# Optimization experiments

Measured on AMD Instinct MI355X. Metric: run time of the kernel, lower is better.

The kernel has to match this reference:

```python
import jax, jax.numpy as jnp
import numpy as np

NUM_COEFF = 32   # num_coeff_per_dim
NUM_POINTS = 64  # Chebyshev collocation points
MAX_ITERS = 10
TOL = 0.01
BATCH, DIM, HID, T_EVAL_N = 512, 256, 512, 16


def T_grid(t, n):
    # Chebyshev T_k(t), k=0..n-1 -> [n, len(t)]
    rows = [jnp.ones_like(t), t]
    for _ in range(2, n):
        rows.append(2.0 * t * rows[-1] - rows[-2])
    return jnp.stack(rows[:n])


def U_grid(t, n):
    rows = [jnp.ones_like(t), 2.0 * t]
    for _ in range(2, n):
        rows.append(2.0 * t * rows[-1] - rows[-2])
    return jnp.stack(rows[:n])


def DT_grid(t, n):
    # d/dt T_k = k * U_{k-1}
    return jnp.vstack([jnp.zeros((1, t.shape[0]), t.dtype),
                       U_grid(t, n - 1) * jnp.arange(1, n, dtype=t.dtype)[:, None]])


def vf_point(t, y, W1, b1, W2, b2):
    # f(t, y) for y [B, D], scalar t
    h = jnp.tanh(y @ W1 + b1 + t)
    return h @ W2 + b2


def vf_grid(t, y, W1, b1, W2, b2):
    # vectorized over Chebyshev points: y [B, D, P], t [P]
    h = jnp.tanh(jnp.einsum('bdp,dh->bhp', y, W1) + b1[None, :, None] + t[None, None, :])
    return jnp.einsum('bhp,hd->bdp', h, W2) + b2[None, :, None]


def setup_inputs() -> dict:
    key = jax.random.key(0)
    ks = jax.random.split(key, 7)
    s1 = 1.0 / np.sqrt(DIM)
    s2 = 1.0 / np.sqrt(HID)
    return {
        'y_init': jax.random.normal(ks[0], (BATCH, DIM), jnp.float32),
        't_eval': jnp.linspace(0.0, 1.0, T_EVAL_N, dtype=jnp.float32),
        'B_init': jax.random.uniform(ks[1], (BATCH, DIM, NUM_COEFF - 2), jnp.float32),
        'W1': jax.random.normal(ks[2], (DIM, HID), jnp.float32) * s1,
        'b1': jax.random.normal(ks[3], (HID,), jnp.float32) * 0.1,
        'W2': jax.random.normal(ks[4], (HID, DIM), jnp.float32) * s2,
        'b2': jax.random.normal(ks[5], (DIM,), jnp.float32) * 0.1,
    }


def _pan_solve(y_init, t_eval, B_init, W1, b1, W2, b2):
    t0, t1 = t_eval[0], t_eval[-1]
    dt = t_eval.dtype
    # time-independent spectral operators
    t_cheb = -jnp.sign(t1 - t0) * jnp.cos(jnp.pi * jnp.arange(NUM_POINTS, dtype=dt) / NUM_POINTS)
    Dt = jnp.diff(jnp.concatenate([t_cheb, jnp.ones((1,), dt)]))
    Phi = T_grid(t_cheb, NUM_COEFF)                        # [N, P]
    DPhi = (2.0 / (t1 - t0)) * DT_grid(t_cheb, NUM_COEFF)  # [N, P]
    inv0 = jnp.linalg.inv(jnp.stack([Phi[0:2, 0], DPhi[0:2, 0]]).T)  # [2,2]
    PD2 = jnp.stack([Phi[2:, 0], DPhi[2:, 0]], axis=-1)    # [N-2, 2]
    D01 = jnp.stack([DPhi[0, :], DPhi[1, :]], axis=0)      # [2, P]
    Phi_b = DPhi[2:, :] - PD2 @ inv0 @ D01                 # [N-2, P]
    Q = jnp.linalg.inv(Phi_b @ (Dt[:, None] * Phi_b.T))    # [N-2, N-2]
    PhibTQ = (Dt[:, None] * Phi_b.T) @ Q                   # [P, N-2]
    M2 = inv0 @ D01 @ PhibTQ                               # [2, N-2]

    f_init = vf_point(t0, y_init, W1, b1, W2, b2)
    yf2 = jnp.stack([y_init, f_init], axis=-1)             # [B, D, 2]

    def head(B_tail):
        return (yf2 - B_tail @ PD2) @ inv0                 # [B, D, 2]

    B = B_init
    done = jnp.array(False)
    delta = jnp.array(jnp.inf, dt)
    iters = jnp.array(0, jnp.int32)
    for _ in range(MAX_ITERS):  # Picard fixed-point iteration (masked early stop)
        B_prev = B
        B_full = jnp.concatenate([head(B_prev), B_prev], axis=-1)  # [B, D, N]
        y_grid = jnp.einsum('bdn,np->bdp', B_full, Phi)            # [B, D, P]
        fapprox = vf_grid(t_cheb, y_grid, W1, b1, W2, b2)          # [B, D, P]
        B_new = jnp.einsum('bdp,pn->bdn', fapprox, PhibTQ) - yf2 @ M2
        d = jnp.linalg.norm(B_new - B_prev)
        B = jnp.where(done, B_prev, B_new)
        delta = jnp.where(done, delta, d)
        iters = jnp.where(done, iters, iters + 1)
        done = done | (d < TOL)

    B_full = jnp.concatenate([head(B), B], axis=-1)
    t_out = -1.0 + 2.0 * (t_eval - t0) / (t1 - t0)
    Phi_out = T_grid(t_out, NUM_COEFF)                     # [N, T]
    traj = jnp.einsum('bdn,nt->tbd', B_full, Phi_out)      # [T, B, D]
    return traj, B, delta, iters


def reference(y_init, t_eval, B_init, W1, b1, W2, b2):
    traj, B, delta, iters = _pan_solve(y_init, t_eval, B_init, W1, b1, W2, b2)
    return (t_eval, traj, delta, B)
```

## Files before the change

### kernel.cpp

```cpp
#include <hip/hip_runtime.h>
#include <math.h>

#define NBATCH 512
#define NDIM 256
#define NHID 512
#define NC 32
#define NTAIL 30
#define NP 64
#define TEV 16
#define MAXIT 10
#define TOLF 0.01f
#define PI_F 3.14159265358979323846f

typedef __bf16 bf16_t;
typedef __bf16 bf16x8 __attribute__((ext_vector_type(8)));
typedef float f32x4 __attribute__((ext_vector_type(4)));
typedef unsigned short ushort_t;

constexpr size_t OFF_TCHEB = 0;
constexpr size_t OFF_PHIT  = 64;
constexpr size_t OFF_PD2I  = 2112;
constexpr size_t OFF_M2    = 2176;
constexpr size_t OFF_INV0  = 2240;
constexpr size_t OFF_PHIOUT= 2256;
constexpr size_t OFF_PQ    = 2768;
constexpr size_t OFF_PQBH  = 4816;
constexpr size_t OFF_PQBL  = 5840;
constexpr size_t OFF_PHIH  = 6864;
constexpr size_t OFF_PHIL  = 7888;
constexpr size_t OFF_SCAL  = 8912;
constexpr size_t OFF_H1F   = 8928;
constexpr size_t OFF_YF2I  = OFF_H1F + 262144;
constexpr size_t OFF_YFR   = OFF_YF2I + 262144;
constexpr size_t OFF_BT    = OFF_YFR + 3932160;
constexpr size_t OFF_W1T   = OFF_BT + 3932160;
constexpr size_t OFF_W2T   = OFF_W1T + 65536;
constexpr size_t WS_FLOATS = OFF_W2T + 65536;

constexpr size_t OUT_TEVAL = 0;
constexpr size_t OUT_TRAJ  = 16;
constexpr size_t OUT_DELTA = 16 + (size_t)TEV*NBATCH*NDIM;
constexpr size_t OUT_B     = OUT_DELTA + 1;

__device__ __forceinline__ ushort_t bf16bits(float v) {
    bf16_t h = (bf16_t)v; ushort_t u; __builtin_memcpy(&u, &h, 2); return u;
}
__device__ __forceinline__ float bf16val(ushort_t u) {
    bf16_t h; __builtin_memcpy(&h, &u, 2); return (float)h;
}

__global__ void setup_kernel(const float* __restrict__ t_eval, float* __restrict__ ws,
                             float* __restrict__ out)
{
    __shared__ float Phi[32][64];
    __shared__ float DPhi[32][64];
    __shared__ float Phib[30][64];
    __shared__ float tcs[64];
    __shared__ float DtS[64];
    __shared__ float inv0s[4];
    __shared__ float pd2s[30][2];
    __shared__ double Gaug[30][61];
    __shared__ double rowk[60];
    __shared__ double colk[30];

    const int tid = threadIdx.x;
    const float t0 = t_eval[0], t1 = t_eval[TEV-1];
    const float sgn = (t1 > t0) ? 1.f : -1.f;

    if (tid < 64) {
        const float t = -sgn * cosf(PI_F * (float)tid / 64.f);
        tcs[tid] = t;
        float p0 = 1.f, p1 = t;
        Phi[0][tid] = p0; Phi[1][tid] = p1;
        for (int k = 2; k < 32; ++k) { float pk = 2.f*t*p1 - p0; Phi[k][tid] = pk; p0 = p1; p1 = pk; }
        const float sc = 2.f / (t1 - t0);
        float u0 = 1.f, u1 = 2.f*t;
        DPhi[0][tid] = 0.f;
        DPhi[1][tid] = sc * 1.f * u0;
        DPhi[2][tid] = sc * 2.f * u1;
        for (int k = 3; k < 32; ++k) { float uk = 2.f*t*u1 - u0; DPhi[k][tid] = sc * (float)k * uk; u0 = u1; u1 = uk; }
    }
    __syncthreads();
    if (tid < 64) DtS[tid] = ((tid < 63) ? tcs[tid+1] : 1.0f) - tcs[tid];
    if (tid == 0) {
        double a = Phi[0][0], b = DPhi[0][0], c = Phi[1][0], d = DPhi[1][0];
        double det = a*d - b*c;
        inv0s[0] = (float)( d/det); inv0s[1] = (float)(-b/det);
        inv0s[2] = (float)(-c/det); inv0s[3] = (float)( a/det);
    }
    __syncthreads();
    if (tid == 0) { ws[OFF_INV0+0]=inv0s[0]; ws[OFF_INV0+1]=inv0s[1]; ws[OFF_INV0+2]=inv0s[2]; ws[OFF_INV0+3]=inv0s[3]; }
    if (tid < 30) {
        float P = Phi[2+tid][0], D = DPhi[2+tid][0];
        float a0 = P*inv0s[0] + D*inv0s[2];
        float a1 = P*inv0s[1] + D*inv0s[3];
        pd2s[tid][0] = a0; pd2s[tid][1] = a1;
        ws[OFF_PD2I + tid*2+0] = a0;
        ws[OFF_PD2I + tid*2+1] = a1;
    }
    __syncthreads();
    if (tid < 64)
        for (int m = 0; m < 30; ++m)
            Phib[m][tid] = DPhi[2+m][tid] - (pd2s[m][0]*DPhi[0][tid] + pd2s[m][1]*DPhi[1][tid]);
    __syncthreads();

    for (int e = tid; e < 900; e += 256) {
        int i = e / 30, j = e % 30;
        double s = 0.0;
        for (int p = 0; p < 64; ++p) s += (double)Phib[i][p] * (double)DtS[p] * (double)Phib[j][p];
        Gaug[i][j] = s;
        Gaug[i][30+j] = (i == j) ? 1.0 : 0.0;
    }
    __syncthreads();

    for (int k = 0; k < 30; ++k) {
        double invpv = 1.0 / Gaug[k][k];
        if (tid < 60) rowk[tid] = Gaug[k][tid] * invpv;
        if (tid >= 64 && tid < 94) colk[tid-64] = Gaug[tid-64][k];
        __syncthreads();
        for (int e = tid; e < 1800; e += 256) {
            int i = e / 60, j = e - i*60;
            if (i == k) Gaug[i][j] = rowk[j];
            else        Gaug[i][j] -= colk[i] * rowk[j];
        }
        __syncthreads();
    }

    if (tid < 64) {
        ushort_t* pqh = (ushort_t*)(ws + OFF_PQBH);
        ushort_t* pql = (ushort_t*)(ws + OFF_PQBL);
        float pqrow[32];
        for (int n = 0; n < 30; ++n) {
            double s = 0.0;
            for (int m = 0; m < 30; ++m) s += (double)Phib[m][tid] * Gaug[m][30+n];
            pqrow[n] = (float)((double)DtS[tid] * s);
        }
        pqrow[30] = 0.f; pqrow[31] = 0.f;
        for (int n = 0; n < 32; ++n) {
            ws[OFF_PQ + (size_t)tid*32 + n] = pqrow[n];
            bf16_t h = (bf16_t)pqrow[n];
            float hf = (float)h;
            pqh[n*64 + tid] = bf16bits(pqrow[n]);
            pql[n*64 + tid] = bf16bits(pqrow[n] - hf);
        }
    }
    __syncthreads();

    if (tid < 30) {
        double a20 = 0.0, a21 = 0.0;
        for (int p = 0; p < 64; ++p) {
            double pq = (double)ws[OFF_PQ + (size_t)p*32 + tid];
            a20 += (double)DPhi[0][p] * pq;
            a21 += (double)DPhi[1][p] * pq;
        }
        ws[OFF_M2 + 0*32 + tid] = (float)((double)inv0s[0]*a20 + (double)inv0s[1]*a21);
        ws[OFF_M2 + 1*32 + tid] = (float)((double)inv0s[2]*a20 + (double)inv0s[3]*a21);
    }

    if (tid < 64) {
        ushort_t* phh = (ushort_t*)(ws + OFF_PHIH);
        ushort_t* phl = (ushort_t*)(ws + OFF_PHIL);
        for (int n = 0; n < 32; ++n) {
            float f = Phi[n][tid];
            ws[OFF_PHIT + (size_t)tid*32 + n] = f;
            ushort_t hb = bf16bits(f);
            phh[tid*32 + n] = hb;
            phl[tid*32 + n] = bf16bits(f - bf16val(hb));
        }
        ws[OFF_TCHEB + tid] = tcs[tid];
    }

    if (tid < TEV) {
        float te = t_eval[tid];
        out[OUT_TEVAL + tid] = te;
        float tt = -1.f + 2.f*(te - t0)/(t1 - t0);
        float q0 = 1.f, q1 = tt;
        ws[OFF_PHIOUT + (size_t)tid*32 + 0] = q0;
        ws[OFF_PHIOUT + (size_t)tid*32 + 1] = q1;
        for (int k = 2; k < 32; ++k) { float qk = 2.f*tt*q1 - q0; ws[OFF_PHIOUT + (size_t)tid*32 + k] = qk; q0 = q1; q1 = qk; }
    }

    if (tid == 0) {
        double* acc = (double*)(ws + OFF_SCAL);
        acc[0] = 0.0;
        int* ip = (int*)(ws + OFF_SCAL + 2);
        ip[0] = 0;
        ip[1] = 0;
    }
}

__global__ __launch_bounds__(256) void transB_kernel(const float* __restrict__ Bin, float* __restrict__ Bt)
{
    const int t = threadIdx.x, b = blockIdx.x;
    const float* src = Bin + ((size_t)(b*NDIM + t)) * NTAIL;
    #pragma unroll
    for (int n = 0; n < NTAIL; ++n)
        Bt[((size_t)b*NTAIL + n)*NDIM + t] = src[n];
}

__global__ __launch_bounds__(256) void transW_kernel(const float* __restrict__ W, bf16_t* __restrict__ Wt,
                                                     int R, int C)
{
    __shared__ float Ls[64][65];
    const int r0 = blockIdx.x*64, c0 = blockIdx.y*64;
    const int lr = threadIdx.x >> 6, lc = threadIdx.x & 63;
    #pragma unroll
    for (int i = 0; i < 16; ++i) {
        int rr = i*4 + lr;
        Ls[rr][lc] = W[(size_t)(r0+rr)*C + c0+lc];
    }
    __syncthreads();
    #pragma unroll
    for (int i = 0; i < 16; ++i) {
        int cc = i*4 + lr;
        Wt[(size_t)(c0+cc)*R + r0 + lc] = (bf16_t)Ls[lc][cc];
    }
}

__global__ __launch_bounds__(512) void finit_h_kernel(const float* __restrict__ y, const float* __restrict__ W1,
                                                      const float* __restrict__ b1, const float* __restrict__ t_eval,
                                                      float* __restrict__ h1)
{
    __shared__ float ys[NDIM];
    const int t = threadIdx.x, b = blockIdx.x;
    if (t < NDIM) ys[t] = y[(size_t)b*NDIM + t];
    __syncthreads();
    float acc = b1[t] + t_eval[0];
    for (int d = 0; d < NDIM; ++d) acc += ys[d] * W1[(size_t)d*NHID + t];
    h1[(size_t)b*NHID + t] = tanhf(acc);
}

__global__ __launch_bounds__(256) void finit_rest_kernel(const float* __restrict__ y, const float* __restrict__ W2,
                                                         const float* __restrict__ b2, const float* __restrict__ h1,
                                                         const float* __restrict__ inv0,
                                                         float* __restrict__ yf2i, float* __restrict__ yfr)
{
    __shared__ float hs[NHID];
    const int t = threadIdx.x, b = blockIdx.x;
    hs[t] = h1[(size_t)b*NHID + t];
    hs[t+256] = h1[(size_t)b*NHID + 256 + t];
    __syncthreads();
    float f = b2[t];
    for (int h = 0; h < NHID; ++h) f += hs[h] * W2[(size_t)h*NDIM + t];
    const float yv = y[(size_t)b*NDIM + t];
    yf2i[((size_t)b*2 + 0)*NDIM + t] = yv*inv0[0] + f*inv0[2];
    yf2i[((size_t)b*2 + 1)*NDIM + t] = yv*inv0[1] + f*inv0[3];
    yfr[((size_t)b*2 + 0)*NDIM + t] = yv;
    yfr[((size_t)b*2 + 1)*NDIM + t] = f;
}

__global__ __launch_bounds__(512, 4) void iter_kernel(
    const float* __restrict__ pd2i, const float* __restrict__ yf2i, const float* __restrict__ tch,
    const bf16_t* __restrict__ W1t, const bf16_t* __restrict__ W2t,
    const float* __restrict__ b1f, const float* __restrict__ b2f,
    const ushort_t* __restrict__ PQhi, const ushort_t* __restrict__ PQlo,
    const ushort_t* __restrict__ phiH, const ushort_t* __restrict__ phiL,
    const float* __restrict__ yfr, const float* __restrict__ M2f,
    float* __restrict__ Bt,
    double* __restrict__ accum, int* __restrict__ counter,
    int* __restrict__ done, float* __restrict__ outDelta)
{
    if (*done) return;
    __shared__ float pd2s[32][2];
    __shared__ float tchS[64];
    __shared__ float m2S[64];
    __shared__ double redd[8];
    __shared__ __align__(16) char smemA[33792];
    __shared__ __align__(16) char smemB[17408];
    __shared__ __align__(16) ushort_t PQHs[32*72];
    __shared__ __align__(16) ushort_t PQLs[32*72];

    const int t = threadIdx.x;
    const int b = blockIdx.x;
    const int lane = t & 63, w = t >> 6;
    const int fr = lane & 15, quad = lane >> 4;

    if (t < 60) ((float*)pd2s)[t] = pd2i[t];
    if (t >= 64 && t < 128) tchS[t-64] = tch[t-64];
    if (t >= 128 && t < 192) m2S[t-128] = M2f[t-128];
    __syncthreads();

    if (t < 256) {
        float cf[32];
        #pragma unroll
        for (int n = 0; n < NTAIL; ++n) cf[2+n] = Bt[((size_t)b*NTAIL + n)*NDIM + t];
        float c0 = yf2i[((size_t)b*2 + 0)*NDIM + t];
        float c1 = yf2i[((size_t)b*2 + 1)*NDIM + t];
        #pragma unroll
        for (int n = 0; n < NTAIL; ++n) { c0 -= cf[2+n]*pd2s[n][0]; c1 -= cf[2+n]*pd2s[n][1]; }
        cf[0] = c0; cf[1] = c1;
        unsigned* BH32 = (unsigned*)smemA;
        unsigned* BL32 = (unsigned*)(smemA + 16384);
        #pragma unroll
        for (int n2 = 0; n2 < 16; ++n2) {
            float f0 = cf[2*n2], f1 = cf[2*n2+1];
            ushort_t h0 = bf16bits(f0), h1 = bf16bits(f1);
            ushort_t l0 = bf16bits(f0 - bf16val(h0)), l1 = bf16bits(f1 - bf16val(h1));
            int idx = t*16 + ((n2 >> 2) ^ (t & 3))*4 + (n2 & 3);
            BH32[idx] = (unsigned)h0 | ((unsigned)h1 << 16);
            BL32[idx] = (unsigned)l0 | ((unsigned)l1 << 16);
        }
    } else {
        int e = (t - 256) * 8;
        int r = e >> 6, c = e & 63;
        uint4 vh = *(const uint4*)(PQhi + e);
        uint4 vl = *(const uint4*)(PQlo + e);
        *(uint4*)(PQHs + r*72 + c) = vh;
        *(uint4*)(PQLs + r*72 + c) = vl;
    }
    __syncthreads();

    ushort_t* Ay = (ushort_t*)smemA;
    {
        bf16x8 bH[2], bL[2];
        const ushort_t* BHu = (const ushort_t*)smemA;
        const ushort_t* BLu = (const ushort_t*)(smemA + 16384);
        #pragma unroll
        for (int j = 0; j < 2; ++j) {
            const int d = w*32 + j*16 + fr;
            const int off = d*32 + (quad ^ (d & 3))*8;
            bH[j] = *(const bf16x8*)(BHu + off);
            bL[j] = *(const bf16x8*)(BLu + off);
        }
        bf16x8 aH[4], aL[4];
        #pragma unroll
        for (int i = 0; i < 4; ++i) {
            aH[i] = *(const bf16x8*)(phiH + (i*16 + fr)*32 + quad*8);
            aL[i] = *(const bf16x8*)(phiL + (i*16 + fr)*32 + quad*8);
        }
        __syncthreads();
        f32x4 accY[4][2];
        #pragma unroll
        for (int i = 0; i < 4; ++i)
            #pragma unroll
            for (int j = 0; j < 2; ++j) {
                f32x4 a = (f32x4){0.f,0.f,0.f,0.f};
                a = __builtin_amdgcn_mfma_f32_16x16x32_bf16(aH[i], bH[j], a, 0, 0, 0);
                a = __builtin_amdgcn_mfma_f32_16x16x32_bf16(aH[i], bL[j], a, 0, 0, 0);
                a = __builtin_amdgcn_mfma_f32_16x16x32_bf16(aL[i], bH[j], a, 0, 0, 0);
                accY[i][j] = a;
            }
        #pragma unroll
        for (int i = 0; i < 4; ++i)
            #pragma unroll
            for (int j = 0; j < 2; ++j)
                #pragma unroll
                for (int r = 0; r < 4; ++r) {
                    const int p = i*16 + quad*4 + r;
                    const int d = w*32 + j*16 + fr;
                    Ay[p*264 + d] = bf16bits(accY[i][j][r]);
                }
    }
    __syncthreads();

    ushort_t* Hc = (ushort_t*)smemB;
    f32x4 accF[4][2];
    #pragma unroll
    for (int i = 0; i < 4; ++i)
        #pragma unroll
        for (int j = 0; j < 2; ++j) accF[i][j] = (f32x4){0.f,0.f,0.f,0.f};

    #pragma unroll
    for (int pass = 0; pass < 4; ++pass) {
        bf16x8 w2f[4][2];
        #pragma unroll
        for (int kt4 = 0; kt4 < 4; ++kt4)
            #pragma unroll
            for (int j = 0; j < 2; ++j) {
                const int d = w*32 + j*16 + fr;
                w2f[kt4][j] = *(const bf16x8*)(W2t + (size_t)d*NHID + pass*128 + kt4*32 + quad*8);
            }
        f32x4 acc1[4];
        #pragma unroll
        for (int i = 0; i < 4; ++i) acc1[i] = (f32x4){0.f,0.f,0.f,0.f};
        #pragma unroll
        for (int kt = 0; kt < NDIM; kt += 32) {
            bf16x8 af[4], bfv;
            #pragma unroll
            for (int i = 0; i < 4; ++i)
                af[i] = *(const bf16x8*)(Ay + (i*16 + fr)*264 + kt + quad*8);
            {
                const int ncol = pass*128 + w*16 + fr;
                bfv = *(const bf16x8*)(W1t + (size_t)ncol*NDIM + kt + quad*8);
            }
            #pragma unroll
            for (int i = 0; i < 4; ++i)
                acc1[i] = __builtin_amdgcn_mfma_f32_16x16x32_bf16(af[i], bfv, acc1[i], 0, 0, 0);
        }
        __syncthreads();
        {
            const int col = w*16 + fr;
            const float bv = b1f[pass*128 + col];
            #pragma unroll
            for (int i = 0; i < 4; ++i)
                #pragma unroll
                for (int r = 0; r < 4; ++r) {
                    const int row = i*16 + quad*4 + r;
                    float v = acc1[i][r] + bv + tchS[row];
                    v = fminf(fmaxf(v, -15.f), 15.f);
                    float e = __expf(2.f*v);
                    Hc[row*136 + col] = bf16bits((e - 1.f)/(e + 1.f));
                }
        }
        __syncthreads();
        #pragma unroll
        for (int kt4 = 0; kt4 < 4; ++kt4) {
            bf16x8 af[4];
            #pragma unroll
            for (int i = 0; i < 4; ++i)
                af[i] = *(const bf16x8*)(Hc + (i*16 + fr)*136 + kt4*32 + quad*8);
            #pragma unroll
            for (int i = 0; i < 4; ++i)
                #pragma unroll
                for (int j = 0; j < 2; ++j)
                    accF[i][j] = __builtin_amdgcn_mfma_f32_16x16x32_bf16(af[i], w2f[kt4][j], accF[i][j], 0, 0, 0);
        }
    }
    __syncthreads();

    {
        unsigned* FsT32 = (unsigned*)smemA;
        #pragma unroll
        for (int i = 0; i < 4; ++i)
            #pragma unroll
            for (int j = 0; j < 2; ++j) {
                const int d = w*32 + j*16 + fr;
                const float bv = b2f[d];
                #pragma unroll
                for (int rp = 0; rp < 2; ++rp) {
                    unsigned u0 = bf16bits(accF[i][j][rp*2]   + bv);
                    unsigned u1 = bf16bits(accF[i][j][rp*2+1] + bv);
                    FsT32[d*33 + i*8 + quad*2 + rp] = u0 | (u1 << 16);
                }
            }
    }
    __syncthreads();

    double ss = 0.0;
    {
        const ushort_t* FsTu = (const ushort_t*)smemA;
        float yvv[2], ffv[2];
        #pragma unroll
        for (int j2 = 0; j2 < 2; ++j2) {
            const int d2 = w*32 + j2*16 + fr;
            yvv[j2] = yfr[((size_t)b*2 + 0)*NDIM + d2];
            ffv[j2] = yfr[((size_t)b*2 + 1)*NDIM + d2];
        }
        f32x4 acc2[2][2];
        #pragma unroll
        for (int m2 = 0; m2 < 2; ++m2)
            #pragma unroll
            for (int j2 = 0; j2 < 2; ++j2) acc2[m2][j2] = (f32x4){0.f,0.f,0.f,0.f};
        #pragma unroll
        for (int kk = 0; kk < 2; ++kk) {
            bf16x8 ah[2], al[2];
            #pragma unroll
            for (int m2 = 0; m2 < 2; ++m2) {
                const int off = (m2*16 + fr)*72 + kk*32 + quad*8;
                ah[m2] = *(const bf16x8*)(PQHs + off);
                al[m2] = *(const bf16x8*)(PQLs + off);
            }
            #pragma unroll
            for (int j2 = 0; j2 < 2; ++j2) {
                const int d2 = w*32 + j2*16 + fr;
                bf16x8 bfv = *(const bf16x8*)(FsTu + d2*66 + kk*32 + quad*8);
                #pragma unroll
                for (int m2 = 0; m2 < 2; ++m2) {
                    acc2[m2][j2] = __builtin_amdgcn_mfma_f32_16x16x32_bf16(ah[m2], bfv, acc2[m2][j2], 0, 0, 0);
                    acc2[m2][j2] = __builtin_amdgcn_mfma_f32_16x16x32_bf16(al[m2], bfv, acc2[m2][j2], 0, 0, 0);
                }
            }
        }
        #pragma unroll
        for (int m2 = 0; m2 < 2; ++m2)
            #pragma unroll
            for (int j2 = 0; j2 < 2; ++j2)
                #pragma unroll
                for (int rr = 0; rr < 4; ++rr) {
                    const int n = m2*16 + quad*4 + rr;
                    if (n < NTAIL) {
                        const int d = w*32 + j2*16 + fr;
                        const size_t idx = ((size_t)b*NTAIL + n)*NDIM + d;
                        float ym2v = yvv[j2]*m2S[n] + ffv[j2]*m2S[32 + n];
                        float val = acc2[m2][j2][rr] - ym2v;
                        float old = Bt[idx];
                        float diff = val - old;
                        Bt[idx] = val;
                        ss += (double)diff*(double)diff;
                    }
                }
    }

    #pragma unroll
    for (int off = 32; off > 0; off >>= 1) ss += __shfl_down(ss, off, 64);
    if (lane == 0) redd[w] = ss;
    __syncthreads();
    if (t == 0) {
        double tot = redd[0] + redd[1] + redd[2] + redd[3]
                   + redd[4] + redd[5] + redd[6] + redd[7];
        atomicAdd(accum, tot);
        __threadfence();
        int old = atomicAdd(counter, 1);
        if (old == 511) {
            unsigned long long raw = atomicExch((unsigned long long*)accum, 0ull);
            double total; __builtin_memcpy(&total, &raw, 8);
            float dl = (float)sqrt(total);
            *outDelta = dl;
            *counter = 0;
            if (dl < TOLF) *done = 1;
        }
    }
}

__global__ __launch_bounds__(256) void kernelEpi(const float* __restrict__ PhiOut, const float* __restrict__ pd2i,
                                                 const float* __restrict__ yf2i, const float* __restrict__ Bt,
                                                 float* __restrict__ outTraj, float* __restrict__ outB)
{
    __shared__ float Po[16][32];
    const int t = threadIdx.x, b = blockIdx.x;
    for (int i = t; i < 512; i += 256) ((float*)Po)[i] = PhiOut[i];
    __syncthreads();
    float cf[32];
    #pragma unroll
    for (int n = 0; n < NTAIL; ++n) cf[2+n] = Bt[((size_t)b*NTAIL + n)*NDIM + t];
    float c0 = yf2i[((size_t)b*2 + 0)*NDIM + t];
    float c1 = yf2i[((size_t)b*2 + 1)*NDIM + t];
    #pragma unroll
    for (int n = 0; n < NTAIL; ++n) { c0 -= cf[2+n]*pd2i[n*2]; c1 -= cf[2+n]*pd2i[n*2+1]; }
    cf[0] = c0; cf[1] = c1;
    for (int tt = 0; tt < TEV; ++tt) {
        float s = 0.f;
        #pragma unroll
        for (int k = 0; k < 32; ++k) s += cf[k]*Po[tt][k];
        outTraj[((size_t)tt*NBATCH + b)*NDIM + t] = s;
    }
    float* ob = outB + ((size_t)(b*NDIM + t))*NTAIL;
    #pragma unroll
    for (int n = 0; n < NTAIL; ++n) ob[n] = cf[2+n];
}

extern "C" void kernel_launch(void* const* d_in, const int* in_sizes, int n_in,
                              void* d_out, int out_size, void* d_ws, size_t ws_size,
                              hipStream_t stream)
{
    const float* y_init = (const float*)d_in[0];
    const float* t_eval = (const float*)d_in[1];
    const float* B_init = (const float*)d_in[2];
    const float* W1     = (const float*)d_in[3];
    const float* b1     = (const float*)d_in[4];
    const float* W2     = (const float*)d_in[5];
    const float* b2     = (const float*)d_in[6];
    float* out = (float*)d_out;
    float* ws  = (float*)d_ws;
    if (ws_size < WS_FLOATS * sizeof(float)) return;

    float* tcheb = ws + OFF_TCHEB;
    float* pd2i  = ws + OFF_PD2I;
    float* M2    = ws + OFF_M2;
    float* inv0  = ws + OFF_INV0;
    float* PhiOut= ws + OFF_PHIOUT;
    double* accum = (double*)(ws + OFF_SCAL);
    int* done    = (int*)(ws + OFF_SCAL + 2);
    int* counter = (int*)(ws + OFF_SCAL + 3);
    float* h1   = ws + OFF_H1F;
    float* yf2i = ws + OFF_YF2I;
    float* yfr  = ws + OFF_YFR;
    float* Bt   = ws + OFF_BT;
    bf16_t* W1t = (bf16_t*)(ws + OFF_W1T);
    bf16_t* W2t = (bf16_t*)(ws + OFF_W2T);
    ushort_t* pqh = (ushort_t*)(ws + OFF_PQBH);
    ushort_t* pql = (ushort_t*)(ws + OFF_PQBL);
    ushort_t* phh = (ushort_t*)(ws + OFF_PHIH);
    ushort_t* phl = (ushort_t*)(ws + OFF_PHIL);

    setup_kernel<<<1, 256, 0, stream>>>(t_eval, ws, out);
    transB_kernel<<<NBATCH, 256, 0, stream>>>(B_init, Bt);
    transW_kernel<<<dim3(NDIM/64, NHID/64), 256, 0, stream>>>(W1, W1t, NDIM, NHID);
    transW_kernel<<<dim3(NHID/64, NDIM/64), 256, 0, stream>>>(W2, W2t, NHID, NDIM);
    finit_h_kernel<<<NBATCH, 512, 0, stream>>>(y_init, W1, b1, t_eval, h1);
    finit_rest_kernel<<<NBATCH, 256, 0, stream>>>(y_init, W2, b2, h1, inv0, yf2i, yfr);

    for (int it = 0; it < MAXIT; ++it) {
        iter_kernel<<<NBATCH, 512, 0, stream>>>(pd2i, yf2i, tcheb, W1t, W2t, b1, b2,
                                                pqh, pql, phh, phl, yfr, M2, Bt,
                                                accum, counter, done, out + OUT_DELTA);
    }
    kernelEpi<<<NBATCH, 256, 0, stream>>>(PhiOut, pd2i, yf2i, Bt, out + OUT_TRAJ, out + OUT_B);
}
```

Baseline: 705.2 us.

## Merge six prologue kernels into one role-dispatched launch

Replaces the setup, B transpose, two weight transposes and the two initial vector-field kernels with a single kernel whose blocks pick a role from blockIdx. The f(t0,y0) evaluation is fused into one block per batch row, and the 2x2 inverse is recomputed in closed form so it no longer waits on the setup block. This removes five launch gaps and the h1 round trip through global memory. In exchange the single setup block, with its serial Gauss-Jordan loop, now runs alongside the other roles, and every block reserves 40 KB of shared memory at 512 threads, which may cut occupancy for the light roles.

```diff
diff --git a/kernel.cpp b/kernel.cpp
--- a/kernel.cpp
+++ b/kernel.cpp
@@ -49,204 +49,217 @@
     bf16_t h; __builtin_memcpy(&h, &u, 2); return (float)h;
 }
 
-__global__ void setup_kernel(const float* __restrict__ t_eval, float* __restrict__ ws,
-                             float* __restrict__ out)
+__global__ __launch_bounds__(512) void prologue_kernel(
+    const float* __restrict__ t_eval, const float* __restrict__ y,
+    const float* __restrict__ Bin,
+    const float* __restrict__ W1, const float* __restrict__ b1,
+    const float* __restrict__ W2, const float* __restrict__ b2,
+    float* __restrict__ ws, float* __restrict__ out)
 {
-    __shared__ float Phi[32][64];
-    __shared__ float DPhi[32][64];
-    __shared__ float Phib[30][64];
-    __shared__ float tcs[64];
-    __shared__ float DtS[64];
-    __shared__ float inv0s[4];
-    __shared__ float pd2s[30][2];
-    __shared__ double Gaug[30][61];
-    __shared__ double rowk[60];
-    __shared__ double colk[30];
+    struct SetupSh {
+        double Gaug[30][61];
+        double rowk[60];
+        double colk[30];
+        float Phi[32][64];
+        float DPhi[32][64];
+        float Phib[30][64];
+        float tcs[64];
+        float DtS[64];
+        float inv0s[4];
+        float pd2s[30][2];
+    };
+    __shared__ __align__(16) char pm[40960];
+    static_assert(sizeof(SetupSh) <= 40960, "SetupSh too big");
 
     const int tid = threadIdx.x;
-    const float t0 = t_eval[0], t1 = t_eval[TEV-1];
-    const float sgn = (t1 > t0) ? 1.f : -1.f;
-
-    if (tid < 64) {
-        const float t = -sgn * cosf(PI_F * (float)tid / 64.f);
-        tcs[tid] = t;
-        float p0 = 1.f, p1 = t;
-        Phi[0][tid] = p0; Phi[1][tid] = p1;
-        for (int k = 2; k < 32; ++k) { float pk = 2.f*t*p1 - p0; Phi[k][tid] = pk; p0 = p1; p1 = pk; }
-        const float sc = 2.f / (t1 - t0);
-        float u0 = 1.f, u1 = 2.f*t;
-        DPhi[0][tid] = 0.f;
-        DPhi[1][tid] = sc * 1.f * u0;
-        DPhi[2][tid] = sc * 2.f * u1;
-        for (int k = 3; k < 32; ++k) { float uk = 2.f*t*u1 - u0; DPhi[k][tid] = sc * (float)k * uk; u0 = u1; u1 = uk; }
-    }
-    __syncthreads();
-    if (tid < 64) DtS[tid] = ((tid < 63) ? tcs[tid+1] : 1.0f) - tcs[tid];
-    if (tid == 0) {
-        double a = Phi[0][0], b = DPhi[0][0], c = Phi[1][0], d = DPhi[1][0];
-        double det = a*d - b*c;
-        inv0s[0] = (float)( d/det); inv0s[1] = (float)(-b/det);
-        inv0s[2] = (float)(-c/det); inv0s[3] = (float)( a/det);
-    }
-    __syncthreads();
-    if (tid == 0) { ws[OFF_INV0+0]=inv0s[0]; ws[OFF_INV0+1]=inv0s[1]; ws[OFF_INV0+2]=inv0s[2]; ws[OFF_INV0+3]=inv0s[3]; }
-    if (tid < 30) {
-        float P = Phi[2+tid][0], D = DPhi[2+tid][0];
-        float a0 = P*inv0s[0] + D*inv0s[2];
-        float a1 = P*inv0s[1] + D*inv0s[3];
-        pd2s[tid][0] = a0; pd2s[tid][1] = a1;
-        ws[OFF_PD2I + tid*2+0] = a0;
-        ws[OFF_PD2I + tid*2+1] = a1;
-    }
-    __syncthreads();
-    if (tid < 64)
-        for (int m = 0; m < 30; ++m)
-            Phib[m][tid] = DPhi[2+m][tid] - (pd2s[m][0]*DPhi[0][tid] + pd2s[m][1]*DPhi[1][tid]);
-    __syncthreads();
-
-    for (int e = tid; e < 900; e += 256) {
-        int i = e / 30, j = e % 30;
-        double s = 0.0;
-        for (int p = 0; p < 64; ++p) s += (double)Phib[i][p] * (double)DtS[p] * (double)Phib[j][p];
-        Gaug[i][j] = s;
-        Gaug[i][30+j] = (i == j) ? 1.0 : 0.0;
-    }
-    __syncthreads();
-
-    for (int k = 0; k < 30; ++k) {
-        double invpv = 1.0 / Gaug[k][k];
-        if (tid < 60) rowk[tid] = Gaug[k][tid] * invpv;
-        if (tid >= 64 && tid < 94) colk[tid-64] = Gaug[tid-64][k];
-        __syncthreads();
-        for (int e = tid; e < 1800; e += 256) {
-            int i = e / 60, j = e - i*60;
-            if (i == k) Gaug[i][j] = rowk[j];
-            else        Gaug[i][j] -= colk[i] * rowk[j];
-        }
-        __syncthreads();
-    }
-
-    if (tid < 64) {
-        ushort_t* pqh = (ushort_t*)(ws + OFF_PQBH);
-        ushort_t* pql = (ushort_t*)(ws + OFF_PQBL);
-        float pqrow[32];
-        for (int n = 0; n < 30; ++n) {
+    const int role = blockIdx.x;
+
+    if (role == 0) {
+        SetupSh& S = *(SetupSh*)pm;
+        const float t0 = t_eval[0], t1 = t_eval[TEV-1];
+        const float sgn = (t1 > t0) ? 1.f : -1.f;
+
+        if (tid < 64) {
+            const float t = -sgn * cosf(PI_F * (float)tid / 64.f);
+            S.tcs[tid] = t;
+            float p0 = 1.f, p1 = t;
+            S.Phi[0][tid] = p0; S.Phi[1][tid] = p1;
+            for (int k = 2; k < 32; ++k) { float pk = 2.f*t*p1 - p0; S.Phi[k][tid] = pk; p0 = p1; p1 = pk; }
+            const float sc = 2.f / (t1 - t0);
+            float u0 = 1.f, u1 = 2.f*t;
+            S.DPhi[0][tid] = 0.f;
+            S.DPhi[1][tid] = sc * 1.f * u0;
+            S.DPhi[2][tid] = sc * 2.f * u1;
+            for (int k = 3; k < 32; ++k) { float uk = 2.f*t*u1 - u0; S.DPhi[k][tid] = sc * (float)k * uk; u0 = u1; u1 = uk; }
+        }
+        __syncthreads();
+        if (tid < 64) S.DtS[tid] = ((tid < 63) ? S.tcs[tid+1] : 1.0f) - S.tcs[tid];
+        if (tid == 0) {
+            double a = S.Phi[0][0], b = S.DPhi[0][0], c = S.Phi[1][0], d = S.DPhi[1][0];
+            double det = a*d - b*c;
+            S.inv0s[0] = (float)( d/det); S.inv0s[1] = (float)(-b/det);
+            S.inv0s[2] = (float)(-c/det); S.inv0s[3] = (float)( a/det);
+        }
+        __syncthreads();
+        if (tid < 30) {
+            float P = S.Phi[2+tid][0], D = S.DPhi[2+tid][0];
+            float a0 = P*S.inv0s[0] + D*S.inv0s[2];
+            float a1 = P*S.inv0s[1] + D*S.inv0s[3];
+            S.pd2s[tid][0] = a0; S.pd2s[tid][1] = a1;
+            ws[OFF_PD2I + tid*2+0] = a0;
+            ws[OFF_PD2I + tid*2+1] = a1;
+        }
+        __syncthreads();
+        if (tid < 64)
+            for (int m = 0; m < 30; ++m)
+                S.Phib[m][tid] = S.DPhi[2+m][tid] - (S.pd2s[m][0]*S.DPhi[0][tid] + S.pd2s[m][1]*S.DPhi[1][tid]);
+        __syncthreads();
+
+        for (int e = tid; e < 900; e += 512) {
+            int i = e / 30, j = e % 30;
             double s = 0.0;
-            for (int m = 0; m < 30; ++m) s += (double)Phib[m][tid] * Gaug[m][30+n];
-            pqrow[n] = (float)((double)DtS[tid] * s);
-        }
-        pqrow[30] = 0.f; pqrow[31] = 0.f;
-        for (int n = 0; n < 32; ++n) {
-            ws[OFF_PQ + (size_t)tid*32 + n] = pqrow[n];
-            bf16_t h = (bf16_t)pqrow[n];
-            float hf = (float)h;
-            pqh[n*64 + tid] = bf16bits(pqrow[n]);
-            pql[n*64 + tid] = bf16bits(pqrow[n] - hf);
-        }
-    }
-    __syncthreads();
-
-    if (tid < 30) {
-        double a20 = 0.0, a21 = 0.0;
-        for (int p = 0; p < 64; ++p) {
-            double pq = (double)ws[OFF_PQ + (size_t)p*32 + tid];
-            a20 += (double)DPhi[0][p] * pq;
-            a21 += (double)DPhi[1][p] * pq;
-        }
-        ws[OFF_M2 + 0*32 + tid] = (float)((double)inv0s[0]*a20 + (double)inv0s[1]*a21);
-        ws[OFF_M2 + 1*32 + tid] = (float)((double)inv0s[2]*a20 + (double)inv0s[3]*a21);
-    }
-
-    if (tid < 64) {
-        ushort_t* phh = (ushort_t*)(ws + OFF_PHIH);
-        ushort_t* phl = (ushort_t*)(ws + OFF_PHIL);
-        for (int n = 0; n < 32; ++n) {
-            float f = Phi[n][tid];
-            ws[OFF_PHIT + (size_t)tid*32 + n] = f;
-            ushort_t hb = bf16bits(f);
-            phh[tid*32 + n] = hb;
-            phl[tid*32 + n] = bf16bits(f - bf16val(hb));
-        }
-        ws[OFF_TCHEB + tid] = tcs[tid];
-    }
-
-    if (tid < TEV) {
-        float te = t_eval[tid];
-        out[OUT_TEVAL + tid] = te;
-        float tt = -1.f + 2.f*(te - t0)/(t1 - t0);
-        float q0 = 1.f, q1 = tt;
-        ws[OFF_PHIOUT + (size_t)tid*32 + 0] = q0;
-        ws[OFF_PHIOUT + (size_t)tid*32 + 1] = q1;
-        for (int k = 2; k < 32; ++k) { float qk = 2.f*tt*q1 - q0; ws[OFF_PHIOUT + (size_t)tid*32 + k] = qk; q0 = q1; q1 = qk; }
-    }
-
-    if (tid == 0) {
-        double* acc = (double*)(ws + OFF_SCAL);
-        acc[0] = 0.0;
-        int* ip = (int*)(ws + OFF_SCAL + 2);
-        ip[0] = 0;
-        ip[1] = 0;
-    }
-}
-
-__global__ __launch_bounds__(256) void transB_kernel(const float* __restrict__ Bin, float* __restrict__ Bt)
-{
-    const int t = threadIdx.x, b = blockIdx.x;
-    const float* src = Bin + ((size_t)(b*NDIM + t)) * NTAIL;
-    #pragma unroll
-    for (int n = 0; n < NTAIL; ++n)
-        Bt[((size_t)b*NTAIL + n)*NDIM + t] = src[n];
-}
-
-__global__ __launch_bounds__(256) void transW_kernel(const float* __restrict__ W, bf16_t* __restrict__ Wt,
-                                                     int R, int C)
-{
-    __shared__ float Ls[64][65];
-    const int r0 = blockIdx.x*64, c0 = blockIdx.y*64;
-    const int lr = threadIdx.x >> 6, lc = threadIdx.x & 63;
-    #pragma unroll
-    for (int i = 0; i < 16; ++i) {
-        int rr = i*4 + lr;
-        Ls[rr][lc] = W[(size_t)(r0+rr)*C + c0+lc];
-    }
-    __syncthreads();
-    #pragma unroll
-    for (int i = 0; i < 16; ++i) {
-        int cc = i*4 + lr;
-        Wt[(size_t)(c0+cc)*R + r0 + lc] = (bf16_t)Ls[lc][cc];
-    }
-}
-
-__global__ __launch_bounds__(512) void finit_h_kernel(const float* __restrict__ y, const float* __restrict__ W1,
-                                                      const float* __restrict__ b1, const float* __restrict__ t_eval,
-                                                      float* __restrict__ h1)
-{
-    __shared__ float ys[NDIM];
-    const int t = threadIdx.x, b = blockIdx.x;
-    if (t < NDIM) ys[t] = y[(size_t)b*NDIM + t];
-    __syncthreads();
-    float acc = b1[t] + t_eval[0];
-    for (int d = 0; d < NDIM; ++d) acc += ys[d] * W1[(size_t)d*NHID + t];
-    h1[(size_t)b*NHID + t] = tanhf(acc);
-}
-
-__global__ __launch_bounds__(256) void finit_rest_kernel(const float* __restrict__ y, const float* __restrict__ W2,
-                                                         const float* __restrict__ b2, const float* __restrict__ h1,
-                                                         const float* __restrict__ inv0,
-                                                         float* __restrict__ yf2i, float* __restrict__ yfr)
-{
-    __shared__ float hs[NHID];
-    const int t = threadIdx.x, b = blockIdx.x;
-    hs[t] = h1[(size_t)b*NHID + t];
-    hs[t+256] = h1[(size_t)b*NHID + 256 + t];
-    __syncthreads();
-    float f = b2[t];
-    for (int h = 0; h < NHID; ++h) f += hs[h] * W2[(size_t)h*NDIM + t];
-    const float yv = y[(size_t)b*NDIM + t];
-    yf2i[((size_t)b*2 + 0)*NDIM + t] = yv*inv0[0] + f*inv0[2];
-    yf2i[((size_t)b*2 + 1)*NDIM + t] = yv*inv0[1] + f*inv0[3];
-    yfr[((size_t)b*2 + 0)*NDIM + t] = yv;
-    yfr[((size_t)b*2 + 1)*NDIM + t] = f;
+            for (int p = 0; p < 64; ++p) s += (double)S.Phib[i][p] * (double)S.DtS[p] * (double)S.Phib[j][p];
+            S.Gaug[i][j] = s;
+            S.Gaug[i][30+j] = (i == j) ? 1.0 : 0.0;
+        }
+        __syncthreads();
+
+        for (int k = 0; k < 30; ++k) {
+            double invpv = 1.0 / S.Gaug[k][k];
+            if (tid < 60) S.rowk[tid] = S.Gaug[k][tid] * invpv;
+            if (tid >= 64 && tid < 94) S.colk[tid-64] = S.Gaug[tid-64][k];
+            __syncthreads();
+            for (int e = tid; e < 1800; e += 512) {
+                int i = e / 60, j = e - i*60;
+                if (i == k) S.Gaug[i][j] = S.rowk[j];
+                else        S.Gaug[i][j] -= S.colk[i] * S.rowk[j];
+            }
+            __syncthreads();
+        }
+
+        if (tid < 64) {
+            ushort_t* pqh = (ushort_t*)(ws + OFF_PQBH);
+            ushort_t* pql = (ushort_t*)(ws + OFF_PQBL);
+            float pqrow[32];
+            for (int n = 0; n < 30; ++n) {
+                double s = 0.0;
+                for (int m = 0; m < 30; ++m) s += (double)S.Phib[m][tid] * S.Gaug[m][30+n];
+                pqrow[n] = (float)((double)S.DtS[tid] * s);
+            }
+            pqrow[30] = 0.f; pqrow[31] = 0.f;
+            for (int n = 0; n < 32; ++n) {
+                ws[OFF_PQ + (size_t)tid*32 + n] = pqrow[n];
+                bf16_t h = (bf16_t)pqrow[n];
+                float hf = (float)h;
+                pqh[n*64 + tid] = bf16bits(pqrow[n]);
+                pql[n*64 + tid] = bf16bits(pqrow[n] - hf);
+            }
+        }
+        __syncthreads();
+
+        if (tid < 30) {
+            double a20 = 0.0, a21 = 0.0;
+            for (int p = 0; p < 64; ++p) {
+                double pq = (double)ws[OFF_PQ + (size_t)p*32 + tid];
+                a20 += (double)S.DPhi[0][p] * pq;
+                a21 += (double)S.DPhi[1][p] * pq;
+            }
+            ws[OFF_M2 + 0*32 + tid] = (float)((double)S.inv0s[0]*a20 + (double)S.inv0s[1]*a21);
+            ws[OFF_M2 + 1*32 + tid] = (float)((double)S.inv0s[2]*a20 + (double)S.inv0s[3]*a21);
+        }
+
+        if (tid < 64) {
+            ushort_t* phh = (ushort_t*)(ws + OFF_PHIH);
+            ushort_t* phl = (ushort_t*)(ws + OFF_PHIL);
+            for (int n = 0; n < 32; ++n) {
+                float f = S.Phi[n][tid];
+                ws[OFF_PHIT + (size_t)tid*32 + n] = f;
+                ushort_t hb = bf16bits(f);
+                phh[tid*32 + n] = hb;
+                phl[tid*32 + n] = bf16bits(f - bf16val(hb));
+            }
+            ws[OFF_TCHEB + tid] = S.tcs[tid];
+        }
+
+        if (tid < TEV) {
+            float te = t_eval[tid];
+            out[OUT_TEVAL + tid] = te;
+            float tt = -1.f + 2.f*(te - t0)/(t1 - t0);
+            float q0 = 1.f, q1 = tt;
+            ws[OFF_PHIOUT + (size_t)tid*32 + 0] = q0;
+            ws[OFF_PHIOUT + (size_t)tid*32 + 1] = q1;
+            for (int k = 2; k < 32; ++k) { float qk = 2.f*tt*q1 - q0; ws[OFF_PHIOUT + (size_t)tid*32 + k] = qk; q0 = q1; q1 = qk; }
+        }
+
+        if (tid == 0) {
+            double* acc = (double*)(ws + OFF_SCAL);
+            acc[0] = 0.0;
+            int* ip = (int*)(ws + OFF_SCAL + 2);
+            ip[0] = 0;
+            ip[1] = 0;
+        }
+    } else if (role <= NBATCH) {
+        const int b = role - 1;
+        float* ys = (float*)pm;
+        float* hs = (float*)pm + 256;
+        if (tid < NDIM) ys[tid] = y[(size_t)b*NDIM + tid];
+        __syncthreads();
+        {
+            float acc = b1[tid] + t_eval[0];
+            for (int d = 0; d < NDIM; ++d) acc += ys[d] * W1[(size_t)d*NHID + tid];
+            hs[tid] = tanhf(acc);
+        }
+        __syncthreads();
+        if (tid < NDIM) {
+            float f = b2[tid];
+            for (int h = 0; h < NHID; ++h) f += hs[h] * W2[(size_t)h*NDIM + tid];
+            const float yv = ys[tid];
+            const float t0 = t_eval[0], t1 = t_eval[TEV-1];
+            const float sgn = (t1 > t0) ? 1.f : -1.f;
+            const float sc = 2.f / (t1 - t0);
+            double a = 1.0, bb = 0.0, c = (double)(-sgn), d = (double)sc;
+            double det = a*d - bb*c;
+            const float i0 = (float)( d/det), i1 = (float)(-bb/det);
+            const float i2 = (float)(-c/det), i3 = (float)( a/det);
+            float* yf2i = ws + OFF_YF2I;
+            float* yfr  = ws + OFF_YFR;
+            yf2i[((size_t)b*2 + 0)*NDIM + tid] = yv*i0 + f*i2;
+            yf2i[((size_t)b*2 + 1)*NDIM + tid] = yv*i1 + f*i3;
+            yfr [((size_t)b*2 + 0)*NDIM + tid] = yv;
+            yfr [((size_t)b*2 + 1)*NDIM + tid] = f;
+        }
+    } else if (role <= 2*NBATCH) {
+        if (tid < NDIM) {
+            const int b = role - NBATCH - 1;
+            float* Bt = ws + OFF_BT;
+            const float* src = Bin + ((size_t)(b*NDIM + tid)) * NTAIL;
+            #pragma unroll
+            for (int n = 0; n < NTAIL; ++n)
+                Bt[((size_t)b*NTAIL + n)*NDIM + tid] = src[n];
+        }
+    } else {
+        const bool isW1 = (role <= 2*NBATCH + 32);
+        const int idx = isW1 ? (role - 2*NBATCH - 1) : (role - 2*NBATCH - 33);
+        const int R = isW1 ? NDIM : NHID;
+        const int C = isW1 ? NHID : NDIM;
+        const float* W = isW1 ? W1 : W2;
+        bf16_t* Wt = (bf16_t*)(ws + (isW1 ? OFF_W1T : OFF_W2T));
+        const int nbx = R / 64;
+        const int r0 = (idx % nbx) * 64, c0 = (idx / nbx) * 64;
+        float (*Ls)[65] = (float(*)[65])pm;
+        const int lr = tid >> 6, lc = tid & 63;
+        #pragma unroll
+        for (int i = 0; i < 8; ++i) {
+            int rr = i*8 + lr;
+            Ls[rr][lc] = W[(size_t)(r0+rr)*C + c0+lc];
+        }
+        __syncthreads();
+        #pragma unroll
+        for (int i = 0; i < 8; ++i) {
+            int cc = i*8 + lr;
+            Wt[(size_t)(c0+cc)*R + r0 + lc] = (bf16_t)Ls[lc][cc];
+        }
+    }
 }
 
 __global__ __launch_bounds__(512, 4) void iter_kernel(
@@ -557,12 +570,10 @@
     float* tcheb = ws + OFF_TCHEB;
     float* pd2i  = ws + OFF_PD2I;
     float* M2    = ws + OFF_M2;
-    float* inv0  = ws + OFF_INV0;
     float* PhiOut= ws + OFF_PHIOUT;
     double* accum = (double*)(ws + OFF_SCAL);
     int* done    = (int*)(ws + OFF_SCAL + 2);
     int* counter = (int*)(ws + OFF_SCAL + 3);
-    float* h1   = ws + OFF_H1F;
     float* yf2i = ws + OFF_YF2I;
     float* yfr  = ws + OFF_YFR;
     float* Bt   = ws + OFF_BT;
@@ -573,12 +584,8 @@
     ushort_t* phh = (ushort_t*)(ws + OFF_PHIH);
     ushort_t* phl = (ushort_t*)(ws + OFF_PHIL);
 
-    setup_kernel<<<1, 256, 0, stream>>>(t_eval, ws, out);
-    transB_kernel<<<NBATCH, 256, 0, stream>>>(B_init, Bt);
-    transW_kernel<<<dim3(NDIM/64, NHID/64), 256, 0, stream>>>(W1, W1t, NDIM, NHID);
-    transW_kernel<<<dim3(NHID/64, NDIM/64), 256, 0, stream>>>(W2, W2t, NHID, NDIM);
-    finit_h_kernel<<<NBATCH, 512, 0, stream>>>(y_init, W1, b1, t_eval, h1);
-    finit_rest_kernel<<<NBATCH, 256, 0, stream>>>(y_init, W2, b2, h1, inv0, yf2i, yfr);
+    prologue_kernel<<<1 + 2*NBATCH + 64, 512, 0, stream>>>(
+        t_eval, y_init, B_init, W1, b1, W2, b2, ws, out);
 
     for (int it = 0; it < MAXIT; ++it) {
         iter_kernel<<<NBATCH, 512, 0, stream>>>(pd2i, yf2i, tcheb, W1t, W2t, b1, b2,
```

New measurement: 666.8 us. 5.4% less time.
